# Kernel tuning notes

Hardware: AMD Instinct MI355X
Metric: run time of the kernel (lower is better)

Reference implementation:

```python
import jax, jax.numpy as jnp
import numpy as np

B, S, D_MODEL, D_QK = 4, 4096, 256, 64


def setup_inputs() -> dict:
    key = jax.random.key(0)
    ks = jax.random.split(key, 6)
    enc_q = jax.random.normal(ks[0], (B, S, D_MODEL), dtype=jnp.float32)
    enc_k = jax.random.normal(ks[1], (B, S, D_MODEL), dtype=jnp.float32)
    enc_v = jax.random.normal(ks[2], (B, S, D_MODEL), dtype=jnp.float32)
    # torch nn.Linear weight layout: [out_features, in_features]
    Wq = jax.random.normal(ks[3], (D_QK, D_MODEL), dtype=jnp.float32) * (D_MODEL ** -0.5)
    Wk = jax.random.normal(ks[4], (D_QK, D_MODEL), dtype=jnp.float32) * (D_MODEL ** -0.5)
    Wv = jax.random.normal(ks[5], (D_MODEL, D_MODEL), dtype=jnp.float32) * (D_MODEL ** -0.5)
    # causal mask: True above the diagonal -> masked out (matches masked_fill semantics)
    mask = jnp.triu(jnp.ones((S, S), dtype=jnp.bool_), k=1)
    return {"encodings_for_q": enc_q, "encodings_for_k": enc_k,
            "encodings_for_v": enc_v, "mask": mask,
            "Wq": Wq, "Wk": Wk, "Wv": Wv}


def reference(encodings_for_q, encodings_for_k, encodings_for_v, mask, Wq, Wk, Wv):
    # linear projections (no bias): x @ W.T
    q = jnp.einsum('bsd,qd->bsq', encodings_for_q, Wq)   # [B,S,d_qk]
    k = jnp.einsum('bsd,qd->bsq', encodings_for_k, Wk)   # [B,S,d_qk]
    v = jnp.einsum('bsd,ed->bse', encodings_for_v, Wv)   # [B,S,d_model]
    scale = k.shape[-1] ** 0.5                            # sqrt(d_qk)
    sims = jnp.einsum('bsq,btq->bst', q, k) / scale       # [B,S,S]
    sims = jnp.where(mask, jnp.float32(-1e9), sims)
    attn = jax.nn.softmax(sims, axis=-1)
    return jnp.einsum('bst,bte->bse', attn, v)            # [B,S,d_model]
```

## Files before the change

kernel.cpp:

```cpp
#include <hip/hip_runtime.h>


#define BATCH 4
#define SEQ   4096
#define DM    256
#define DQK   64

typedef __bf16 bf16x8 __attribute__((ext_vector_type(8)));
typedef float  f32x16 __attribute__((ext_vector_type(16)));

__device__ __forceinline__ unsigned int rnd16(unsigned int u) {
    return u + 0x7fffu + ((u >> 16) & 1u);
}
__device__ __forceinline__ unsigned short f2bf(float f) {
    return (unsigned short)(rnd16(__builtin_bit_cast(unsigned int, f)) >> 16);
}
__device__ __forceinline__ unsigned int pk2bf(float lo, float hi) {
    unsigned int a = rnd16(__builtin_bit_cast(unsigned int, lo));
    unsigned int b = rnd16(__builtin_bit_cast(unsigned int, hi));
    return (a >> 16) | (b & 0xffff0000u);
}
__device__ __forceinline__ bf16x8 u4bf(uint4 u) { return __builtin_bit_cast(bf16x8, u); }

__device__ __forceinline__ void repack_store(const f32x16& acc, int q2, int l,
                                             uint4* __restrict__ out, size_t tile_ofs_u4) {
    unsigned int d0[4], d1[4], p0[4], p1[4];
#pragma unroll
    for (int h = 0; h < 4; ++h) {
        d0[h] = pk2bf(acc[4*h + 0], acc[4*h + 1]);
        d1[h] = pk2bf(acc[4*h + 2], acc[4*h + 3]);
        p0[h] = __shfl_xor((int)d0[h], 32);
        p1[h] = __shfl_xor((int)d1[h], 32);
    }
#pragma unroll
    for (int kc = 0; kc < 2; ++kc) {
        int h = 2*kc + q2;
        uint4 v = (q2 == 0) ? make_uint4(d0[h], d1[h], p0[h], p1[h])
                            : make_uint4(p0[h], p1[h], d0[h], d1[h]);
        out[tile_ofs_u4 + (size_t)kc * 64 + l] = v;
    }
}

__device__ __forceinline__ int obase(int T) {
    return (T < 24) ? (T - 12) : 12 + (T - 24) * 2;
}
__device__ __forceinline__ int dbase(int T) {
    return (T < 24) ? (T - 12) * 2 : 24 + (T - 24) * 3;
}

__global__ __launch_bounds__(256) void proj(const float* __restrict__ Xq,
                                            const float* __restrict__ Xk,
                                            const float* __restrict__ Xv,
                                            const float* __restrict__ Wq,
                                            const float* __restrict__ Wk,
                                            const float* __restrict__ Wv,
                                            uint4* __restrict__ qf,
                                            uint4* __restrict__ kf,
                                            uint4* __restrict__ vf) {
    __shared__ unsigned short Xs[64][264];
    __shared__ unsigned short Ws[64][264];

    const int z = blockIdx.z;
    const int bx = blockIdx.x, b = blockIdx.y;
    const float* X = (z == 0) ? Xq : (z == 1) ? Xk : Xv;
    const float* W = (z == 0) ? Wq : (z == 1) ? Wk : Wv;
    const int s0 = bx * 64;
    const int tid = threadIdx.x, w = tid >> 6, l = tid & 63, ln = l & 31, q2 = l >> 5;

#pragma unroll
    for (int i = 0; i < 16; ++i) {
        int f = i * 256 + tid;
        int r = f >> 6, c4 = f & 63;
        float4 xv = *(const float4*)&X[((size_t)b * SEQ + s0 + r) * DM + c4 * 4];
        ushort4 h; h.x = f2bf(xv.x); h.y = f2bf(xv.y); h.z = f2bf(xv.z); h.w = f2bf(xv.w);
        *(ushort4*)&Xs[r][c4 * 4] = h;
    }

    if (z < 2) {
#pragma unroll
        for (int i = 0; i < 16; ++i) {
            int f = i * 256 + tid;
            int r = f >> 6, c4 = f & 63;
            float4 wv = *(const float4*)&W[(size_t)r * DM + c4 * 4];
            ushort4 h; h.x = f2bf(wv.x); h.y = f2bf(wv.y); h.z = f2bf(wv.z); h.w = f2bf(wv.w);
            *(ushort4*)&Ws[r][c4 * 4] = h;
        }
        __syncthreads();
        const int msub = w >> 1, nsub = w & 1;
        f32x16 a0 = {}, a1 = {};
#pragma unroll
        for (int c = 0; c < 16; c += 2) {
            bf16x8 af0 = u4bf(*(const uint4*)&Ws[msub*32 + ln][c*16 + q2*8]);
            bf16x8 bf0 = u4bf(*(const uint4*)&Xs[nsub*32 + ln][c*16 + q2*8]);
            a0 = __builtin_amdgcn_mfma_f32_32x32x16_bf16(af0, bf0, a0, 0, 0, 0);
            bf16x8 af1 = u4bf(*(const uint4*)&Ws[msub*32 + ln][(c+1)*16 + q2*8]);
            bf16x8 bf1 = u4bf(*(const uint4*)&Xs[nsub*32 + ln][(c+1)*16 + q2*8]);
            a1 = __builtin_amdgcn_mfma_f32_32x32x16_bf16(af1, bf1, a1, 0, 0, 0);
        }
        f32x16 acc = a0 + a1;
        size_t base = (((size_t)(b*128 + bx*2 + nsub)) * 4 + 2*msub) * 64;
        repack_store(acc, q2, l, (z == 0) ? qf : kf, base);
    } else {
        const int msub = w & 1, nsub = w >> 1;
        for (int ecl = 0; ecl < 2; ++ecl) {
            const int ec = (z - 2) * 2 + ecl;
            __syncthreads();
#pragma unroll
            for (int i = 0; i < 16; ++i) {
                int f = i * 256 + tid;
                int r = f >> 6, c4 = f & 63;
                float4 wv = *(const float4*)&W[(size_t)(ec*64 + r) * DM + c4 * 4];
                ushort4 h; h.x = f2bf(wv.x); h.y = f2bf(wv.y); h.z = f2bf(wv.z); h.w = f2bf(wv.w);
                *(ushort4*)&Ws[r][c4 * 4] = h;
            }
            __syncthreads();
            f32x16 a0 = {}, a1 = {};
#pragma unroll
            for (int c = 0; c < 16; c += 2) {
                bf16x8 af0 = u4bf(*(const uint4*)&Xs[msub*32 + ln][c*16 + q2*8]);
                bf16x8 bf0 = u4bf(*(const uint4*)&Ws[nsub*32 + ln][c*16 + q2*8]);
                a0 = __builtin_amdgcn_mfma_f32_32x32x16_bf16(af0, bf0, a0, 0, 0, 0);
                bf16x8 af1 = u4bf(*(const uint4*)&Xs[msub*32 + ln][(c+1)*16 + q2*8]);
                bf16x8 bf1 = u4bf(*(const uint4*)&Ws[nsub*32 + ln][(c+1)*16 + q2*8]);
                a1 = __builtin_amdgcn_mfma_f32_32x32x16_bf16(af1, bf1, a1, 0, 0, 0);
            }
            f32x16 acc = a0 + a1;
            int et = ec*2 + nsub;
            size_t base = (((size_t)(b*8 + et)) * 256 + (size_t)bx*4 + msub*2) * 64;
            repack_store(acc, q2, l, vf, base);
        }
    }
}

__global__ __launch_bounds__(512, 2) void attn(const uint4* __restrict__ qf,
                                               const uint4* __restrict__ kf,
                                               const uint4* __restrict__ vf,
                                               float* __restrict__ out,
                                               unsigned short* __restrict__ Op,
                                               float* __restrict__ Dp) {
    __shared__ uint4 Pb[2][4][8][64];
    __shared__ float denp[8][2][64];
    __shared__ float dfin[128];

    const int bid = blockIdx.x;
    const int slot = bid & 7, u = bid >> 3;
    const int b = slot >> 1;
    const int task = u * 2 + (slot & 1);
    int T, cc, nc;
    if (task < 12)      { T = task;                cc = 0;               nc = 1; }
    else if (task < 36) { int q = task - 12; T = 12 + (q >> 1); cc = q & 1;       nc = 2; }
    else                { int q = task - 36; T = 24 + q / 3;    cc = q - 3*(q/3); nc = 3; }
    const int n = T + 1;
    const int j0 = cc * n / nc, j1 = (cc + 1) * n / nc;

    const int tid = threadIdx.x, w = tid >> 6, l = tid & 63, ln = l & 31, q2 = l >> 5;
    const int ks = w & 3, qp = w >> 2;
    const float cfac = 0.18033688011112042f;

    bf16x8 qv[2][4];
#pragma unroll
    for (int g = 0; g < 2; ++g)
#pragma unroll
        for (int c = 0; c < 4; ++c)
            qv[g][c] = u4bf(qf[(((size_t)b*128 + T*4 + qp*2 + g) * 4 + c) * 64 + l]);

    f32x16 oa[4] = {};
    float den[2] = {0.f, 0.f};

    uint4 kaf[4];
#pragma unroll
    for (int c = 0; c < 4; ++c)
        kaf[c] = kf[(((size_t)b*128 + j0*4 + ks) * 4 + c) * 64 + l];

    for (int jt = j0; jt < j1; ++jt) {
        const int buf = jt & 1;
        const bool diag = (jt == T);

        uint4 vbs[8];
#pragma unroll
        for (int kc = 0; kc < 8; ++kc)
            vbs[kc] = vf[(((size_t)b*8 + w) * 256 + (size_t)jt*8 + kc) * 64 + l];

        f32x16 s0 = {}, s1 = {};
#pragma unroll
        for (int c = 0; c < 4; ++c) {
            bf16x8 ka = u4bf(kaf[c]);
            s0 = __builtin_amdgcn_mfma_f32_32x32x16_bf16(ka, qv[0][c], s0, 0, 0, 0);
            s1 = __builtin_amdgcn_mfma_f32_32x32x16_bf16(ka, qv[1][c], s1, 0, 0, 0);
        }
#pragma unroll
        for (int g = 0; g < 2; ++g) {
            const f32x16 s = g ? s1 : s0;
            const int qsub = qp*2 + g;
            float pv[16], pd = 0.f;
#pragma unroll
            for (int r = 0; r < 16; ++r) {
                float e = __builtin_exp2f(s[r] * cfac);
                if (diag) {
                    int klocal = 4*q2 + (r & 3) + 8*(r >> 2);
                    if (ks*32 + klocal > qsub*32 + ln) e = 0.f;
                }
                pv[r] = e; pd += e;
            }
            den[g] += pd;
#pragma unroll
            for (int quad = 0; quad < 4; ++quad) {
                unsigned int lo = pk2bf(pv[4*quad + 0], pv[4*quad + 1]);
                unsigned int hi = pk2bf(pv[4*quad + 2], pv[4*quad + 3]);
                int kcg = ks*2 + (quad >> 1);
                int h   = quad & 1;
                char* dst = (char*)&Pb[buf][qsub][kcg][h*32 + ln] + q2*8;
                *(uint2*)dst = make_uint2(lo, hi);
            }
        }
        __syncthreads();
        if (jt + 1 < j1) {
#pragma unroll
            for (int c = 0; c < 4; ++c)
                kaf[c] = kf[(((size_t)b*128 + (jt+1)*4 + ks) * 4 + c) * 64 + l];
        }
#pragma unroll
        for (int kc = 0; kc < 8; ++kc) {
            bf16x8 vb = u4bf(vbs[kc]);
#pragma unroll
            for (int qs = 0; qs < 4; ++qs) {
                bf16x8 pa = u4bf(Pb[buf][qs][kc][l]);
                oa[qs] = __builtin_amdgcn_mfma_f32_32x32x16_bf16(pa, vb, oa[qs], 0, 0, 0);
            }
        }
    }

    denp[w][0][l] = den[0];
    denp[w][1][l] = den[1];
    __syncthreads();
    if (tid < 128) {
        int qsub = tid >> 5, qln = tid & 31;
        int g = qsub & 1, wp = qsub >> 1;
        float sden = 0.f;
#pragma unroll
        for (int k4 = 0; k4 < 4; ++k4)
#pragma unroll
            for (int hh = 0; hh < 2; ++hh)
                sden += denp[wp*4 + k4][g][hh*32 + qln];
        dfin[tid] = (nc == 1) ? 1.0f / sden : sden;
    }
    __syncthreads();

    if (nc == 1) {
#pragma unroll
        for (int qs = 0; qs < 4; ++qs)
#pragma unroll
            for (int r = 0; r < 16; ++r) {
                int qrow = qs*32 + (r & 3) + 8*(r >> 2) + 4*q2;
                out[((size_t)b*SEQ + T*128 + qrow) * DM + w*32 + ln] = oa[qs][r] * dfin[qrow];
            }
    } else if (cc == 0) {
#pragma unroll
        for (int qs = 0; qs < 4; ++qs)
#pragma unroll
            for (int r = 0; r < 16; ++r) {
                int qrow = qs*32 + (r & 3) + 8*(r >> 2) + 4*q2;
                out[((size_t)b*SEQ + T*128 + qrow) * DM + w*32 + ln] = oa[qs][r];
            }
        if (tid < 128) Dp[((size_t)b*48 + dbase(T)) * 128 + tid] = dfin[tid];
    } else {
        size_t pidx = (size_t)b*28 + obase(T) + (cc - 1);
#pragma unroll
        for (int qs = 0; qs < 4; ++qs)
#pragma unroll
            for (int r = 0; r < 16; ++r) {
                int qrow = qs*32 + (r & 3) + 8*(r >> 2) + 4*q2;
                Op[(pidx*128 + qrow) * DM + w*32 + ln] = f2bf(oa[qs][r]);
            }
        if (tid < 128) Dp[((size_t)b*48 + dbase(T) + cc) * 128 + tid] = dfin[tid];
    }
}

__global__ __launch_bounds__(256) void combine(const unsigned short* __restrict__ Op,
                                               const float* __restrict__ Dp,
                                               float* __restrict__ out) {
    const int T = 12 + blockIdx.x, b = blockIdx.y, qq = blockIdx.z;
    const int nc = (T < 24) ? 2 : 3;
    const int t = threadIdx.x;
    const size_t db = (size_t)b*48 + dbase(T);
    const size_t pb = (size_t)b*28 + obase(T);
#pragma unroll 4
    for (int r = 0; r < 32; ++r) {
        int q = qq*32 + r;
        size_t oofs = ((size_t)b*SEQ + T*128 + q) * DM + t;
        float sum = out[oofs];
        float dsum = 0.f;
        for (int c = 0; c < nc; ++c) dsum += Dp[(db + c)*128 + q];
        for (int c = 1; c < nc; ++c) {
            unsigned int uv = Op[((pb + c - 1)*128 + q) * DM + t];
            sum += __builtin_bit_cast(float, uv << 16);
        }
        out[oofs] = sum / dsum;
    }
}

extern "C" void kernel_launch(void* const* d_in, const int* in_sizes, int n_in,
                              void* d_out, int out_size, void* d_ws, size_t ws_size,
                              hipStream_t stream) {
    const float* enc_q = (const float*)d_in[0];
    const float* enc_k = (const float*)d_in[1];
    const float* enc_v = (const float*)d_in[2];
    const float* Wq = (const float*)d_in[4];
    const float* Wk = (const float*)d_in[5];
    const float* Wv = (const float*)d_in[6];
    float* out = (float*)d_out;

    uint4* qf = (uint4*)d_ws;
    uint4* kf = qf + 131072;
    uint4* vf = kf + 131072;
    unsigned short* Op = (unsigned short*)(vf + 524288);
    float* Dp = (float*)(Op + (size_t)4*28*128*256);

    proj<<<dim3(64, 4, 4), 256, 0, stream>>>(enc_q, enc_k, enc_v, Wq, Wk, Wv, qf, kf, vf);
    attn<<<240, 512, 0, stream>>>(qf, kf, vf, out, Op, Dp);
    combine<<<dim3(20, 4, 4), 256, 0, stream>>>(Op, Dp, out);
}
```

Measured before the change: 207.3 us.

## Warp-specialize attention: producer waves compute P, consumer waves accumulate PV

Splits the 8 waves of the attention block into four producer waves and four consumer waves. Producers compute QK^T, exp and the denominators for all four query subtiles and write P into a double-buffered LDS tile. Consumers run the PV MFMAs on the previous tile, each covering two output column slices, while V loads for the next tile are issued. The aim is to overlap softmax/exp work with PV matrix math across a one-tile software pipeline. The cost is more registers per consumer wave (two sets of accumulators and V fragments) and idle producers or consumers when the pipeline fills and drains.

```diff
diff --git a/kernel.cpp b/kernel.cpp
--- a/kernel.cpp
+++ b/kernel.cpp
@@ -139,7 +139,7 @@
                                                unsigned short* __restrict__ Op,
                                                float* __restrict__ Dp) {
     __shared__ uint4 Pb[2][4][8][64];
-    __shared__ float denp[8][2][64];
+    __shared__ float denp[4][4][64];
     __shared__ float dfin[128];
 
     const int bid = blockIdx.x;
@@ -154,125 +154,175 @@
     const int j0 = cc * n / nc, j1 = (cc + 1) * n / nc;
 
     const int tid = threadIdx.x, w = tid >> 6, l = tid & 63, ln = l & 31, q2 = l >> 5;
-    const int ks = w & 3, qp = w >> 2;
     const float cfac = 0.18033688011112042f;
 
-    bf16x8 qv[2][4];
-#pragma unroll
-    for (int g = 0; g < 2; ++g)
+    if (w < 4) {
+        const int ks = w;
+        bf16x8 qv[4][4];
+#pragma unroll
+        for (int qs = 0; qs < 4; ++qs)
+#pragma unroll
+            for (int c = 0; c < 4; ++c)
+                qv[qs][c] = u4bf(qf[(((size_t)b*128 + T*4 + qs) * 4 + c) * 64 + l]);
+
+        uint4 kaf[4];
 #pragma unroll
         for (int c = 0; c < 4; ++c)
-            qv[g][c] = u4bf(qf[(((size_t)b*128 + T*4 + qp*2 + g) * 4 + c) * 64 + l]);
-
-    f32x16 oa[4] = {};
-    float den[2] = {0.f, 0.f};
-
-    uint4 kaf[4];
-#pragma unroll
-    for (int c = 0; c < 4; ++c)
-        kaf[c] = kf[(((size_t)b*128 + j0*4 + ks) * 4 + c) * 64 + l];
-
-    for (int jt = j0; jt < j1; ++jt) {
-        const int buf = jt & 1;
-        const bool diag = (jt == T);
-
-        uint4 vbs[8];
-#pragma unroll
-        for (int kc = 0; kc < 8; ++kc)
-            vbs[kc] = vf[(((size_t)b*8 + w) * 256 + (size_t)jt*8 + kc) * 64 + l];
-
-        f32x16 s0 = {}, s1 = {};
-#pragma unroll
-        for (int c = 0; c < 4; ++c) {
-            bf16x8 ka = u4bf(kaf[c]);
-            s0 = __builtin_amdgcn_mfma_f32_32x32x16_bf16(ka, qv[0][c], s0, 0, 0, 0);
-            s1 = __builtin_amdgcn_mfma_f32_32x32x16_bf16(ka, qv[1][c], s1, 0, 0, 0);
-        }
-#pragma unroll
-        for (int g = 0; g < 2; ++g) {
-            const f32x16 s = g ? s1 : s0;
-            const int qsub = qp*2 + g;
-            float pv[16], pd = 0.f;
-#pragma unroll
-            for (int r = 0; r < 16; ++r) {
-                float e = __builtin_exp2f(s[r] * cfac);
-                if (diag) {
-                    int klocal = 4*q2 + (r & 3) + 8*(r >> 2);
-                    if (ks*32 + klocal > qsub*32 + ln) e = 0.f;
+            kaf[c] = kf[(((size_t)b*128 + j0*4 + ks) * 4 + c) * 64 + l];
+
+        float den[4] = {0.f, 0.f, 0.f, 0.f};
+
+        for (int jt = j0; jt < j1; ++jt) {
+            const int buf = jt & 1;
+            const bool diag = (jt == T);
+#pragma unroll
+            for (int g2 = 0; g2 < 2; ++g2) {
+                f32x16 s0 = {}, s1 = {};
+#pragma unroll
+                for (int c = 0; c < 4; ++c) {
+                    bf16x8 ka = u4bf(kaf[c]);
+                    s0 = __builtin_amdgcn_mfma_f32_32x32x16_bf16(ka, qv[2*g2+0][c], s0, 0, 0, 0);
+                    s1 = __builtin_amdgcn_mfma_f32_32x32x16_bf16(ka, qv[2*g2+1][c], s1, 0, 0, 0);
                 }
-                pv[r] = e; pd += e;
-            }
-            den[g] += pd;
-#pragma unroll
-            for (int quad = 0; quad < 4; ++quad) {
-                unsigned int lo = pk2bf(pv[4*quad + 0], pv[4*quad + 1]);
-                unsigned int hi = pk2bf(pv[4*quad + 2], pv[4*quad + 3]);
-                int kcg = ks*2 + (quad >> 1);
-                int h   = quad & 1;
-                char* dst = (char*)&Pb[buf][qsub][kcg][h*32 + ln] + q2*8;
-                *(uint2*)dst = make_uint2(lo, hi);
-            }
-        }
-        __syncthreads();
-        if (jt + 1 < j1) {
-#pragma unroll
-            for (int c = 0; c < 4; ++c)
-                kaf[c] = kf[(((size_t)b*128 + (jt+1)*4 + ks) * 4 + c) * 64 + l];
-        }
-#pragma unroll
-        for (int kc = 0; kc < 8; ++kc) {
-            bf16x8 vb = u4bf(vbs[kc]);
-#pragma unroll
-            for (int qs = 0; qs < 4; ++qs) {
-                bf16x8 pa = u4bf(Pb[buf][qs][kc][l]);
-                oa[qs] = __builtin_amdgcn_mfma_f32_32x32x16_bf16(pa, vb, oa[qs], 0, 0, 0);
-            }
-        }
-    }
-
-    denp[w][0][l] = den[0];
-    denp[w][1][l] = den[1];
-    __syncthreads();
-    if (tid < 128) {
-        int qsub = tid >> 5, qln = tid & 31;
-        int g = qsub & 1, wp = qsub >> 1;
-        float sden = 0.f;
-#pragma unroll
-        for (int k4 = 0; k4 < 4; ++k4)
-#pragma unroll
-            for (int hh = 0; hh < 2; ++hh)
-                sden += denp[wp*4 + k4][g][hh*32 + qln];
-        dfin[tid] = (nc == 1) ? 1.0f / sden : sden;
-    }
-    __syncthreads();
-
-    if (nc == 1) {
-#pragma unroll
-        for (int qs = 0; qs < 4; ++qs)
-#pragma unroll
-            for (int r = 0; r < 16; ++r) {
-                int qrow = qs*32 + (r & 3) + 8*(r >> 2) + 4*q2;
-                out[((size_t)b*SEQ + T*128 + qrow) * DM + w*32 + ln] = oa[qs][r] * dfin[qrow];
-            }
-    } else if (cc == 0) {
-#pragma unroll
-        for (int qs = 0; qs < 4; ++qs)
-#pragma unroll
-            for (int r = 0; r < 16; ++r) {
-                int qrow = qs*32 + (r & 3) + 8*(r >> 2) + 4*q2;
-                out[((size_t)b*SEQ + T*128 + qrow) * DM + w*32 + ln] = oa[qs][r];
-            }
-        if (tid < 128) Dp[((size_t)b*48 + dbase(T)) * 128 + tid] = dfin[tid];
+#pragma unroll
+                for (int g = 0; g < 2; ++g) {
+                    const f32x16 s = g ? s1 : s0;
+                    const int qsub = 2*g2 + g;
+                    float pv[16], pd = 0.f;
+#pragma unroll
+                    for (int r = 0; r < 16; ++r) {
+                        float e = __builtin_exp2f(s[r] * cfac);
+                        if (diag) {
+                            int klocal = 4*q2 + (r & 3) + 8*(r >> 2);
+                            if (ks*32 + klocal > qsub*32 + ln) e = 0.f;
+                        }
+                        pv[r] = e; pd += e;
+                    }
+                    den[qsub] += pd;
+#pragma unroll
+                    for (int quad = 0; quad < 4; ++quad) {
+                        unsigned int lo = pk2bf(pv[4*quad + 0], pv[4*quad + 1]);
+                        unsigned int hi = pk2bf(pv[4*quad + 2], pv[4*quad + 3]);
+                        int kcg = ks*2 + (quad >> 1);
+                        int h   = quad & 1;
+                        char* dst = (char*)&Pb[buf][qsub][kcg][h*32 + ln] + q2*8;
+                        *(uint2*)dst = make_uint2(lo, hi);
+                    }
+                }
+            }
+            if (jt + 1 < j1) {
+#pragma unroll
+                for (int c = 0; c < 4; ++c)
+                    kaf[c] = kf[(((size_t)b*128 + (jt+1)*4 + ks) * 4 + c) * 64 + l];
+            }
+            __syncthreads();
+        }
+#pragma unroll
+        for (int qs = 0; qs < 4; ++qs) denp[ks][qs][l] = den[qs];
+        __syncthreads();
+        if (tid < 128) {
+            int qsub = tid >> 5, qln = tid & 31;
+            float sden = 0.f;
+#pragma unroll
+            for (int p = 0; p < 4; ++p)
+#pragma unroll
+                for (int hh = 0; hh < 2; ++hh)
+                    sden += denp[p][qsub][hh*32 + qln];
+            dfin[tid] = (nc == 1) ? 1.0f / sden : sden;
+        }
+        __syncthreads();
+        if (nc > 1 && tid < 128)
+            Dp[((size_t)b*48 + dbase(T) + cc) * 128 + tid] = dfin[tid];
     } else {
-        size_t pidx = (size_t)b*28 + obase(T) + (cc - 1);
-#pragma unroll
-        for (int qs = 0; qs < 4; ++qs)
-#pragma unroll
-            for (int r = 0; r < 16; ++r) {
-                int qrow = qs*32 + (r & 3) + 8*(r >> 2) + 4*q2;
-                Op[(pidx*128 + qrow) * DM + w*32 + ln] = f2bf(oa[qs][r]);
-            }
-        if (tid < 128) Dp[((size_t)b*48 + dbase(T) + cc) * 128 + tid] = dfin[tid];
+        const int cw = w - 4;
+        uint4 vbs[2][8];
+        f32x16 oa[2][4] = {};
+        for (int jt = j0; jt < j1; ++jt) {
+            if (jt == j0) {
+#pragma unroll
+                for (int e = 0; e < 2; ++e)
+#pragma unroll
+                    for (int kc = 0; kc < 8; ++kc)
+                        vbs[e][kc] = vf[(((size_t)b*8 + (2*cw+e)) * 256 + (size_t)j0*8 + kc) * 64 + l];
+            } else {
+                const int buf = (jt - 1) & 1;
+#pragma unroll
+                for (int kc = 0; kc < 8; ++kc) {
+                    bf16x8 pa[4];
+#pragma unroll
+                    for (int qs = 0; qs < 4; ++qs)
+                        pa[qs] = u4bf(Pb[buf][qs][kc][l]);
+#pragma unroll
+                    for (int e = 0; e < 2; ++e) {
+                        bf16x8 vb = u4bf(vbs[e][kc]);
+#pragma unroll
+                        for (int qs = 0; qs < 4; ++qs)
+                            oa[e][qs] = __builtin_amdgcn_mfma_f32_32x32x16_bf16(pa[qs], vb, oa[e][qs], 0, 0, 0);
+                    }
+#pragma unroll
+                    for (int e = 0; e < 2; ++e)
+                        vbs[e][kc] = vf[(((size_t)b*8 + (2*cw+e)) * 256 + (size_t)jt*8 + kc) * 64 + l];
+                }
+            }
+            __syncthreads();
+        }
+        __syncthreads();
+        {
+            const int buf = (j1 - 1) & 1;
+#pragma unroll
+            for (int kc = 0; kc < 8; ++kc) {
+                bf16x8 pa[4];
+#pragma unroll
+                for (int qs = 0; qs < 4; ++qs)
+                    pa[qs] = u4bf(Pb[buf][qs][kc][l]);
+#pragma unroll
+                for (int e = 0; e < 2; ++e) {
+                    bf16x8 vb = u4bf(vbs[e][kc]);
+#pragma unroll
+                    for (int qs = 0; qs < 4; ++qs)
+                        oa[e][qs] = __builtin_amdgcn_mfma_f32_32x32x16_bf16(pa[qs], vb, oa[e][qs], 0, 0, 0);
+                }
+            }
+        }
+        __syncthreads();
+        if (nc == 1) {
+#pragma unroll
+            for (int e = 0; e < 2; ++e) {
+                const int et = 2*cw + e;
+#pragma unroll
+                for (int qs = 0; qs < 4; ++qs)
+#pragma unroll
+                    for (int r = 0; r < 16; ++r) {
+                        int qrow = qs*32 + (r & 3) + 8*(r >> 2) + 4*q2;
+                        out[((size_t)b*SEQ + T*128 + qrow) * DM + et*32 + ln] = oa[e][qs][r] * dfin[qrow];
+                    }
+            }
+        } else if (cc == 0) {
+#pragma unroll
+            for (int e = 0; e < 2; ++e) {
+                const int et = 2*cw + e;
+#pragma unroll
+                for (int qs = 0; qs < 4; ++qs)
+#pragma unroll
+                    for (int r = 0; r < 16; ++r) {
+                        int qrow = qs*32 + (r & 3) + 8*(r >> 2) + 4*q2;
+                        out[((size_t)b*SEQ + T*128 + qrow) * DM + et*32 + ln] = oa[e][qs][r];
+                    }
+            }
+        } else {
+            size_t pidx = (size_t)b*28 + obase(T) + (cc - 1);
+#pragma unroll
+            for (int e = 0; e < 2; ++e) {
+                const int et = 2*cw + e;
+#pragma unroll
+                for (int qs = 0; qs < 4; ++qs)
+#pragma unroll
+                    for (int r = 0; r < 16; ++r) {
+                        int qrow = qs*32 + (r & 3) + 8*(r >> 2) + 4*q2;
+                        Op[(pidx*128 + qrow) * DM + et*32 + ln] = f2bf(oa[e][qs][r]);
+                    }
+            }
+        }
     }
 }
 
```

Result: slower. 235.7 us (+13.7%).

## Split each attention query tile into two 64-row halves across blocks

Applied to the files above, without the earlier changes.

Each attention block now covers 64 query rows instead of 128, and the grid doubles from 240 to 480 blocks. Each wave computes one S tile and two output accumulators instead of two and four, which lowers register and shared-memory use and gives more blocks to spread over the CUs. The cost is that every K and V tile is loaded twice, once per query half, so global/L2 traffic rises and each block has fewer MFMAs to hide its load latency.

```diff
diff --git a/kernel.cpp b/kernel.cpp
--- a/kernel.cpp
+++ b/kernel.cpp
@@ -138,14 +138,14 @@
                                                float* __restrict__ out,
                                                unsigned short* __restrict__ Op,
                                                float* __restrict__ Dp) {
-    __shared__ uint4 Pb[2][4][8][64];
-    __shared__ float denp[8][2][64];
-    __shared__ float dfin[128];
+    __shared__ uint4 Pb[2][2][8][64];
+    __shared__ float denp[4][2][64];
+    __shared__ float dfin[64];
 
     const int bid = blockIdx.x;
-    const int slot = bid & 7, u = bid >> 3;
-    const int b = slot >> 1;
-    const int task = u * 2 + (slot & 1);
+    const int slot = bid & 7;
+    const int b = slot >> 1, qh = slot & 1;
+    const int task = bid >> 3;
     int T, cc, nc;
     if (task < 12)      { T = task;                cc = 0;               nc = 1; }
     else if (task < 36) { int q = task - 12; T = 12 + (q >> 1); cc = q & 1;       nc = 2; }
@@ -154,18 +154,18 @@
     const int j0 = cc * n / nc, j1 = (cc + 1) * n / nc;
 
     const int tid = threadIdx.x, w = tid >> 6, l = tid & 63, ln = l & 31, q2 = l >> 5;
-    const int ks = w & 3, qp = w >> 2;
+    const int ks = w & 3, qg = w >> 2;
+    const int qsub = qh * 2 + qg;
+    const int et = w;
     const float cfac = 0.18033688011112042f;
 
-    bf16x8 qv[2][4];
-#pragma unroll
-    for (int g = 0; g < 2; ++g)
-#pragma unroll
-        for (int c = 0; c < 4; ++c)
-            qv[g][c] = u4bf(qf[(((size_t)b*128 + T*4 + qp*2 + g) * 4 + c) * 64 + l]);
-
-    f32x16 oa[4] = {};
-    float den[2] = {0.f, 0.f};
+    bf16x8 qv[4];
+#pragma unroll
+    for (int c = 0; c < 4; ++c)
+        qv[c] = u4bf(qf[(((size_t)b*128 + T*4 + qsub) * 4 + c) * 64 + l]);
+
+    f32x16 oa[2] = {};
+    float den = 0.f;
 
     uint4 kaf[4];
 #pragma unroll
@@ -179,39 +179,32 @@
         uint4 vbs[8];
 #pragma unroll
         for (int kc = 0; kc < 8; ++kc)
-            vbs[kc] = vf[(((size_t)b*8 + w) * 256 + (size_t)jt*8 + kc) * 64 + l];
-
-        f32x16 s0 = {}, s1 = {};
-#pragma unroll
-        for (int c = 0; c < 4; ++c) {
-            bf16x8 ka = u4bf(kaf[c]);
-            s0 = __builtin_amdgcn_mfma_f32_32x32x16_bf16(ka, qv[0][c], s0, 0, 0, 0);
-            s1 = __builtin_amdgcn_mfma_f32_32x32x16_bf16(ka, qv[1][c], s1, 0, 0, 0);
-        }
-#pragma unroll
-        for (int g = 0; g < 2; ++g) {
-            const f32x16 s = g ? s1 : s0;
-            const int qsub = qp*2 + g;
-            float pv[16], pd = 0.f;
-#pragma unroll
-            for (int r = 0; r < 16; ++r) {
-                float e = __builtin_exp2f(s[r] * cfac);
-                if (diag) {
-                    int klocal = 4*q2 + (r & 3) + 8*(r >> 2);
-                    if (ks*32 + klocal > qsub*32 + ln) e = 0.f;
-                }
-                pv[r] = e; pd += e;
-            }
-            den[g] += pd;
-#pragma unroll
-            for (int quad = 0; quad < 4; ++quad) {
-                unsigned int lo = pk2bf(pv[4*quad + 0], pv[4*quad + 1]);
-                unsigned int hi = pk2bf(pv[4*quad + 2], pv[4*quad + 3]);
-                int kcg = ks*2 + (quad >> 1);
-                int h   = quad & 1;
-                char* dst = (char*)&Pb[buf][qsub][kcg][h*32 + ln] + q2*8;
-                *(uint2*)dst = make_uint2(lo, hi);
-            }
+            vbs[kc] = vf[(((size_t)b*8 + et) * 256 + (size_t)jt*8 + kc) * 64 + l];
+
+        f32x16 s = {};
+#pragma unroll
+        for (int c = 0; c < 4; ++c)
+            s = __builtin_amdgcn_mfma_f32_32x32x16_bf16(u4bf(kaf[c]), qv[c], s, 0, 0, 0);
+
+        float pv[16], pd = 0.f;
+#pragma unroll
+        for (int r = 0; r < 16; ++r) {
+            float e = __builtin_exp2f(s[r] * cfac);
+            if (diag) {
+                int klocal = 4*q2 + (r & 3) + 8*(r >> 2);
+                if (ks*32 + klocal > qsub*32 + ln) e = 0.f;
+            }
+            pv[r] = e; pd += e;
+        }
+        den += pd;
+#pragma unroll
+        for (int quad = 0; quad < 4; ++quad) {
+            unsigned int lo = pk2bf(pv[4*quad + 0], pv[4*quad + 1]);
+            unsigned int hi = pk2bf(pv[4*quad + 2], pv[4*quad + 3]);
+            int kcg = ks*2 + (quad >> 1);
+            int h   = quad & 1;
+            char* dst = (char*)&Pb[buf][qg][kcg][h*32 + ln] + q2*8;
+            *(uint2*)dst = make_uint2(lo, hi);
         }
         __syncthreads();
         if (jt + 1 < j1) {
@@ -223,56 +216,54 @@
         for (int kc = 0; kc < 8; ++kc) {
             bf16x8 vb = u4bf(vbs[kc]);
 #pragma unroll
-            for (int qs = 0; qs < 4; ++qs) {
-                bf16x8 pa = u4bf(Pb[buf][qs][kc][l]);
-                oa[qs] = __builtin_amdgcn_mfma_f32_32x32x16_bf16(pa, vb, oa[qs], 0, 0, 0);
-            }
-        }
-    }
-
-    denp[w][0][l] = den[0];
-    denp[w][1][l] = den[1];
+            for (int qsl = 0; qsl < 2; ++qsl) {
+                bf16x8 pa = u4bf(Pb[buf][qsl][kc][l]);
+                oa[qsl] = __builtin_amdgcn_mfma_f32_32x32x16_bf16(pa, vb, oa[qsl], 0, 0, 0);
+            }
+        }
+    }
+
+    denp[ks][qg][l] = den;
     __syncthreads();
-    if (tid < 128) {
-        int qsub = tid >> 5, qln = tid & 31;
-        int g = qsub & 1, wp = qsub >> 1;
+    if (tid < 64) {
+        int qgl = tid >> 5, qln = tid & 31;
         float sden = 0.f;
 #pragma unroll
-        for (int k4 = 0; k4 < 4; ++k4)
+        for (int p = 0; p < 4; ++p)
 #pragma unroll
             for (int hh = 0; hh < 2; ++hh)
-                sden += denp[wp*4 + k4][g][hh*32 + qln];
+                sden += denp[p][qgl][hh*32 + qln];
         dfin[tid] = (nc == 1) ? 1.0f / sden : sden;
     }
     __syncthreads();
 
     if (nc == 1) {
 #pragma unroll
-        for (int qs = 0; qs < 4; ++qs)
+        for (int qsl = 0; qsl < 2; ++qsl)
 #pragma unroll
             for (int r = 0; r < 16; ++r) {
-                int qrow = qs*32 + (r & 3) + 8*(r >> 2) + 4*q2;
-                out[((size_t)b*SEQ + T*128 + qrow) * DM + w*32 + ln] = oa[qs][r] * dfin[qrow];
+                int qrow = qsl*32 + (r & 3) + 8*(r >> 2) + 4*q2;
+                out[((size_t)b*SEQ + T*128 + qh*64 + qrow) * DM + et*32 + ln] = oa[qsl][r] * dfin[qrow];
             }
     } else if (cc == 0) {
 #pragma unroll
-        for (int qs = 0; qs < 4; ++qs)
+        for (int qsl = 0; qsl < 2; ++qsl)
 #pragma unroll
             for (int r = 0; r < 16; ++r) {
-                int qrow = qs*32 + (r & 3) + 8*(r >> 2) + 4*q2;
-                out[((size_t)b*SEQ + T*128 + qrow) * DM + w*32 + ln] = oa[qs][r];
-            }
-        if (tid < 128) Dp[((size_t)b*48 + dbase(T)) * 128 + tid] = dfin[tid];
+                int qrow = qsl*32 + (r & 3) + 8*(r >> 2) + 4*q2;
+                out[((size_t)b*SEQ + T*128 + qh*64 + qrow) * DM + et*32 + ln] = oa[qsl][r];
+            }
+        if (tid < 64) Dp[((size_t)b*48 + dbase(T)) * 128 + qh*64 + tid] = dfin[tid];
     } else {
         size_t pidx = (size_t)b*28 + obase(T) + (cc - 1);
 #pragma unroll
-        for (int qs = 0; qs < 4; ++qs)
+        for (int qsl = 0; qsl < 2; ++qsl)
 #pragma unroll
             for (int r = 0; r < 16; ++r) {
-                int qrow = qs*32 + (r & 3) + 8*(r >> 2) + 4*q2;
-                Op[(pidx*128 + qrow) * DM + w*32 + ln] = f2bf(oa[qs][r]);
-            }
-        if (tid < 128) Dp[((size_t)b*48 + dbase(T) + cc) * 128 + tid] = dfin[tid];
+                int qrow = qsl*32 + (r & 3) + 8*(r >> 2) + 4*q2;
+                Op[(pidx*128 + qh*64 + qrow) * DM + et*32 + ln] = f2bf(oa[qsl][r]);
+            }
+        if (tid < 64) Dp[((size_t)b*48 + dbase(T) + cc) * 128 + qh*64 + tid] = dfin[tid];
     }
 }
 
@@ -317,6 +308,6 @@
     float* Dp = (float*)(Op + (size_t)4*28*128*256);
 
     proj<<<dim3(64, 4, 4), 256, 0, stream>>>(enc_q, enc_k, enc_v, Wq, Wk, Wv, qf, kf, vf);
-    attn<<<240, 512, 0, stream>>>(qf, kf, vf, out, Op, Dp);
+    attn<<<480, 512, 0, stream>>>(qf, kf, vf, out, Op, Dp);
     combine<<<dim3(20, 4, 4), 256, 0, stream>>>(Op, Dp, out);
 }
```

Result: no change. 208.7 us (+0.7%).
